# Performance work log

Measured on AMD Instinct MI355X. Metric: run time of the kernel, lower is better.

Reference implementation:

```python
import jax, jax.numpy as jnp
import numpy as np

P, NH, KEEP, TOPK = 16, 8, 0.25, 2


def _sincos_1d(embed_dim, pos):
    omega = np.arange(embed_dim // 2, dtype=np.float64)
    omega /= embed_dim / 2.0
    omega = 1.0 / 10000 ** omega
    out = np.einsum('m,d->md', pos.reshape(-1), omega)
    return np.concatenate([np.sin(out), np.cos(out)], axis=1)


def _sincos_2d(embed_dim, gh, gw):
    grid_h = np.arange(gh, dtype=np.float32)
    grid_w = np.arange(gw, dtype=np.float32)
    grid = np.stack(np.meshgrid(grid_w, grid_h), axis=0).reshape(2, -1)
    emb_h = _sincos_1d(embed_dim // 2, grid[0])  # matches original (uses grid[0])
    emb_w = _sincos_1d(embed_dim // 2, grid[1])
    return np.concatenate([emb_h, emb_w], axis=1).astype(np.float32)


def _ln(x, w, b):
    m = x.mean(-1, keepdims=True)
    v = jnp.mean((x - m) ** 2, axis=-1, keepdims=True)
    return (x - m) * jax.lax.rsqrt(v + 1e-5) * w + b


def _mha(q, kv, in_w, in_b, out_w, out_b, nh):
    D = q.shape[-1]
    dh = D // nh
    wq, wk, wv = jnp.split(in_w, 3, 0)
    bq, bk, bv = jnp.split(in_b, 3, 0)
    qq = (q @ wq.T + bq).reshape(q.shape[0], q.shape[1], nh, dh)
    kk = (kv @ wk.T + bk).reshape(kv.shape[0], kv.shape[1], nh, dh)
    vv = (kv @ wv.T + bv).reshape(kv.shape[0], kv.shape[1], nh, dh)
    att = jax.nn.softmax(jnp.einsum('bqhd,bkhd->bhqk', qq, kk) / jnp.sqrt(jnp.asarray(dh, qq.dtype)), -1)
    o = jnp.einsum('bhqk,bkhd->bqhd', att, vv).reshape(q.shape)
    return o @ out_w.T + out_b


def _moe(x, rw, rb, w1, b1, w2, b2):
    E = w1.shape[0]
    probs = jax.nn.softmax(jnp.einsum('btd,ed->bte', x, rw) + rb, -1)
    tv, ti = jax.lax.top_k(probs, TOPK)
    tw = jax.nn.softmax(tv, -1)
    comb = jnp.sum(jax.nn.one_hot(ti, E, dtype=x.dtype) * tw[..., None], axis=-2)  # [B,T,E]
    y = jnp.zeros_like(x)
    for e in range(E):  # small fixed expert count
        h = jax.nn.gelu(jnp.einsum('btd,fd->btf', x, w1[e]) + b1[e], approximate=False)
        o = jnp.einsum('btf,df->btd', h, w2[e]) + b2[e]
        y = y + comb[..., e:e + 1] * o
    return y


def reference(images, type_ids, noise, conv_w, conv_b, latents, type_emb,
              ca_in_w, ca_in_b, ca_out_w, ca_out_b, ca_ln_w, ca_ln_b,
              blk_in_w, blk_in_b, blk_out_w, blk_out_b,
              blk_ln1_w, blk_ln1_b, blk_ln2_w, blk_ln2_b,
              router_w, router_b, e_w1, e_b1, e_w2, e_b2):
    B, _, Hi, Wi = images.shape
    D = conv_w.shape[0]
    x = jax.lax.conv_general_dilated(images, conv_w, (P, P), 'VALID',
                                     dimension_numbers=('NCHW', 'OIHW', 'NCHW'))
    x = x + conv_b[None, :, None, None]
    gh, gw = Hi // P, Wi // P
    patches = x.reshape(B, D, gh * gw).transpose(0, 2, 1)  # [B,N,D]
    patches = patches + jnp.asarray(_sincos_2d(D, gh, gw))[None] + type_emb[type_ids][:, None, :]
    n = patches.shape[1]
    n_vis = max(1, int(n * KEEP))
    ids_shuffle = jnp.argsort(noise, axis=1)
    ids_keep = ids_shuffle[:, :n_vis]
    ids_mask = ids_shuffle[:, n_vis:]
    visible = jnp.take_along_axis(patches, ids_keep[..., None], axis=1)
    lat = jnp.broadcast_to(latents[None], (B,) + latents.shape)
    lat = _ln(lat + _mha(lat, visible, ca_in_w, ca_in_b, ca_out_w, ca_out_b, NH), ca_ln_w, ca_ln_b)
    L = blk_in_w.shape[0]
    for l in range(L):
        lat = _ln(lat + _mha(lat, lat, blk_in_w[l], blk_in_b[l], blk_out_w[l], blk_out_b[l], NH),
                  blk_ln1_w[l], blk_ln1_b[l])
        lat = _ln(lat + _moe(lat, router_w[l], router_b[l], e_w1[l], e_b1[l], e_w2[l], e_b2[l]),
                  blk_ln2_w[l], blk_ln2_b[l])
    return lat, ids_keep, ids_mask


def setup_inputs():
    key = jax.random.key(0)
    B, D, E, L, V = 4, 768, 8, 6, 1000
    ks = iter(jax.random.split(key, 32))

    def nrm(shape, s=0.02):
        return jax.random.normal(next(ks), shape, jnp.float32) * s

    return {
        'images': jax.random.normal(next(ks), (B, 3, 224, 224), jnp.float32),
        'type_ids': jax.random.randint(next(ks), (B,), 0, V),
        'noise': jax.random.uniform(next(ks), (B, 196), jnp.float32),
        'conv_w': nrm((D, 3, P, P)), 'conv_b': jnp.zeros((D,), jnp.float32),
        'latents': jax.random.normal(next(ks), (256, D), jnp.float32),
        'type_emb': nrm((V, D)),
        'ca_in_w': nrm((3 * D, D)), 'ca_in_b': jnp.zeros((3 * D,), jnp.float32),
        'ca_out_w': nrm((D, D)), 'ca_out_b': jnp.zeros((D,), jnp.float32),
        'ca_ln_w': jnp.ones((D,), jnp.float32), 'ca_ln_b': jnp.zeros((D,), jnp.float32),
        'blk_in_w': nrm((L, 3 * D, D)), 'blk_in_b': jnp.zeros((L, 3 * D), jnp.float32),
        'blk_out_w': nrm((L, D, D)), 'blk_out_b': jnp.zeros((L, D), jnp.float32),
        'blk_ln1_w': jnp.ones((L, D), jnp.float32), 'blk_ln1_b': jnp.zeros((L, D), jnp.float32),
        'blk_ln2_w': jnp.ones((L, D), jnp.float32), 'blk_ln2_b': jnp.zeros((L, D), jnp.float32),
        'router_w': nrm((L, E, D)), 'router_b': jnp.zeros((L, E), jnp.float32),
        'e_w1': nrm((L, E, 2 * D, D)), 'e_b1': jnp.zeros((L, E, 2 * D), jnp.float32),
        'e_w2': nrm((L, E, D, 2 * D)), 'e_b2': jnp.zeros((L, E, D), jnp.float32),
    }
```

## Files before the change

### kernel.cpp

```cpp
#include <hip/hip_runtime.h>
#include <math.h>


namespace {

typedef unsigned short u16;
constexpr int Dm  = 768;
constexpr int ML  = 256;
constexpr int BB  = 4;
constexpr int NP  = 196;
constexpr int NV  = 49;
constexpr int NE  = 8;
constexpr int FH_ = 1536;
constexpr int NL  = 6;
constexpr int NT  = 1024;

typedef __attribute__((ext_vector_type(8))) short bf16x8;
typedef __attribute__((ext_vector_type(4))) float f32x4;

__device__ __forceinline__ u16 f2bf(float f){
  union { float f; unsigned u; } v; v.f = f;
  unsigned r = v.u + 0x7fffu + ((v.u >> 16) & 1u);
  return (u16)(r >> 16);
}
__device__ __forceinline__ void pack8(const float4& a, const float4& b, bf16x8& w){
  w[0]=(short)f2bf(a.x); w[1]=(short)f2bf(a.y); w[2]=(short)f2bf(a.z); w[3]=(short)f2bf(a.w);
  w[4]=(short)f2bf(b.x); w[5]=(short)f2bf(b.y); w[6]=(short)f2bf(b.z); w[7]=(short)f2bf(b.w);
}
__device__ __forceinline__ void gload16(const void* g, void* l){
  __builtin_amdgcn_global_load_lds(
      (const __attribute__((address_space(1))) unsigned int*)g,
      (__attribute__((address_space(3))) unsigned int*)l, 16, 0, 0);
}

__device__ __forceinline__ float blk_sum(float v, float* sh){
#pragma unroll
  for (int off = 32; off; off >>= 1) v += __shfl_xor(v, off);
  int wid = threadIdx.x >> 6;
  if ((threadIdx.x & 63) == 0) sh[wid] = v;
  __syncthreads();
  v = sh[0] + sh[1] + sh[2] + sh[3];
  __syncthreads();
  return v;
}

__global__ __launch_bounds__(256) void prologue_k(
    const float* __restrict__ noise, int* __restrict__ ids,
    float* __restrict__ out_keep, float* __restrict__ out_mask,
    const float* __restrict__ images, u16* __restrict__ viscol,
    const float* __restrict__ s0, const float* __restrict__ s1,
    const float* __restrict__ s2, const float* __restrict__ s3,
    const float* __restrict__ s4, const float* __restrict__ s5,
    u16* __restrict__ d0, u16* __restrict__ d1, u16* __restrict__ d2,
    u16* __restrict__ d3, u16* __restrict__ d4, u16* __restrict__ d5)
{
  int bx = blockIdx.x, tid = threadIdx.x;
  __shared__ float shv[NP];
  __shared__ int shord[NP];
  if (bx < 4){
    int b = bx;
    if (tid < NP) shv[tid] = noise[b * NP + tid];
    __syncthreads();
    if (tid < NP){
      float x = shv[tid];
      int rank = 0;
      for (int j = 0; j < NP; j++){
        float y = shv[j];
        rank += (y < x) || (y == x && j < tid);
      }
      shord[rank] = tid;
    }
    __syncthreads();
    if (tid < NP){
      int id = shord[tid];
      ids[b * NP + tid] = id;
      if (tid < NV) out_keep[b * NV + tid] = (float)id;
      else          out_mask[b * (NP - NV) + (tid - NV)] = (float)id;
    }
    return;
  }
  if (bx < 200){
    int bv = bx - 4;
    int b = bv / NV, vq = bv % NV;
    if (tid < NP) shv[tid] = noise[b * NP + tid];
    __syncthreads();
    if (tid < NP){
      float x = shv[tid];
      int rank = 0;
      for (int j = 0; j < NP; j++){
        float y = shv[j];
        rank += (y < x) || (y == x && j < tid);
      }
      if (rank == vq) shord[0] = tid;
    }
    __syncthreads();
    int pid = shord[0];
    int ph = pid / 14, pw = pid % 14;
    int kh = tid >> 4, kw = tid & 15;
#pragma unroll
    for (int c = 0; c < 3; c++)
      viscol[(long)bv * Dm + c * 256 + tid] =
        f2bf(images[((b * 3 + c) * 224 + ph * 16 + kh) * 224 + pw * 16 + kw]);
    return;
  }
  const long c0 = 147456, c1 = 589824, c2 = 737280, c3 = 3391488, c4 = 4276224, c5 = 4325376;
  long i = (long)(bx - 200) * 256 + tid;
  long stride = (long)(gridDim.x - 200) * 256;
  for (; i < c5; i += stride){
    const float* s; u16* d; long off;
    if      (i < c0){ s = s0; d = d0; off = i; }
    else if (i < c1){ s = s1; d = d1; off = i - c0; }
    else if (i < c2){ s = s2; d = d2; off = i - c1; }
    else if (i < c3){ s = s3; d = d3; off = i - c2; }
    else if (i < c4){ s = s4; d = d4; off = i - c3; }
    else            { s = s5; d = d5; off = i - c4; }
    float4 v = *(const float4*)(s + off * 4);
    ushort4 o;
    o.x = f2bf(v.x); o.y = f2bf(v.y); o.z = f2bf(v.z); o.w = f2bf(v.w);
    *(ushort4*)(d + off * 4) = o;
  }
}

template<int MTILE, bool BF16B, bool MOE, bool GATHER, bool POSTYPE>
__global__ __launch_bounds__(256) void g2_k(
    const u16* __restrict__ A, int lda,
    const void* __restrict__ Bv, int ldb, long bSB,
    const float* __restrict__ bias, long biasE,
    float* __restrict__ Cf, u16* __restrict__ Cb, int ldc,
    int M, int N, int K, int act,
    const int* __restrict__ counts, const int* __restrict__ offsets,
    const int* __restrict__ ptok, int mbPerE,
    const int* __restrict__ ids, const int* __restrict__ type_ids,
    const float* __restrict__ type_emb)
{
  constexpr int AF = MTILE / 64;
  constexpr int MF = MTILE / 32;
  __shared__ __align__(16) short lsa[2][MTILE * 32];
  __shared__ __align__(16) short lsb[2][4096];
  int t = threadIdx.x, lane = t & 63, wid = t >> 6;
  int n0 = blockIdx.x << 7;
  int m0, cnt = 0, off = 0;
  const u16* B16 = (const u16*)Bv;
  const float* B32 = (const float*)Bv;
  const float* bb = bias;
  if (MOE){
    int e = blockIdx.y / mbPerE, mb = blockIdx.y - e * mbPerE;
    cnt = counts[e]; m0 = mb * MTILE;
    if (m0 >= cnt) return;
    off = offsets[e];
    if (BF16B) B16 += (long)e * bSB; else B32 += (long)e * bSB;
    bb += (long)e * biasE;
  } else {
    m0 = blockIdx.y * MTILE;
  }

  long aoff[AF];
#pragma unroll
  for (int i = 0; i < AF; i++){
    int idx = i * 256 + t, c = idx / MTILE, r = idx % MTILE;
    int gl = m0 + r;
    long row;
    if (MOE) row = (gl < cnt) ? (GATHER ? (long)ptok[off + gl] : (long)(off + gl))
                              : (GATHER ? (long)ptok[off] : (long)off);
    else     row = (gl < M) ? gl : 0;
    aoff[i] = row * (long)lda + c * 8;
  }
  long boff[2] = {0, 0};
  int bcol = 0, bkh = 0;
  const float* b32p = nullptr;
  if (BF16B){
#pragma unroll
    for (int i = 0; i < 2; i++){
      int idx = i * 256 + t, c = idx >> 7, r = idx & 127;
      int gc = n0 + r; if (gc >= N) gc = 0;
      boff[i] = (long)gc * ldb + c * 8;
    }
  } else {
    bcol = t >> 1; bkh = (t & 1) << 4;
    int gc = n0 + bcol; if (gc >= N) gc = N - 1;
    b32p = B32 + (long)gc * ldb + bkh;
  }

  float4 br[4];
  auto stage = [&](int buf, int k0){
#pragma unroll
    for (int i = 0; i < AF; i++)
      gload16(A + aoff[i] + k0, &lsa[buf][(i * 256 + wid * 64) * 8]);
    if (BF16B){
#pragma unroll
      for (int i = 0; i < 2; i++)
        gload16(B16 + boff[i] + k0, &lsb[buf][(i * 256 + wid * 64) * 8]);
    } else {
#pragma unroll
      for (int j = 0; j < 4; j++) br[j] = *(const float4*)(b32p + k0 + j * 4);
    }
  };
  auto bwrite = [&](int buf){
    if (!BF16B){
      bf16x8 w0, w1;
      pack8(br[0], br[1], w0); pack8(br[2], br[3], w1);
      int c0 = bkh >> 3;
      *(bf16x8*)&lsb[buf][((c0    ) * 128 + bcol) * 8] = w0;
      *(bf16x8*)&lsb[buf][((c0 + 1) * 128 + bcol) * 8] = w1;
    }
  };

  f32x4 acc[MF][4];
#pragma unroll
  for (int m = 0; m < MF; m++)
#pragma unroll
    for (int n = 0; n < 4; n++) acc[m][n] = (f32x4){0.f,0.f,0.f,0.f};

  int T = K >> 5;
  stage(0, 0);
  bwrite(0);
  __syncthreads();

  int wr = wid >> 1, wc = wid & 1, fr = lane & 15, lk = lane >> 4;
  for (int tt = 0; tt < T; tt++){
    int cur = tt & 1, nxt = cur ^ 1;
    if (tt + 1 < T) stage(nxt, (tt + 1) << 5);
    bf16x8 av[MF], bv[4];
#pragma unroll
    for (int m = 0; m < MF; m++)
      av[m] = *(const bf16x8*)&lsa[cur][(lk * MTILE + wr * (MTILE / 2) + m * 16 + fr) * 8];
#pragma unroll
    for (int n = 0; n < 4; n++)
      bv[n] = *(const bf16x8*)&lsb[cur][(lk * 128 + wc * 64 + n * 16 + fr) * 8];
#pragma unroll
    for (int m = 0; m < MF; m++)
#pragma unroll
      for (int n = 0; n < 4; n++)
        acc[m][n] = __builtin_amdgcn_mfma_f32_16x16x32_bf16(av[m], bv[n], acc[m][n], 0, 0, 0);
    if (tt + 1 < T) bwrite(nxt);
    __syncthreads();
  }

#pragma unroll
  for (int m = 0; m < MF; m++)
#pragma unroll
  for (int i = 0; i < 4; i++){
    int rl = m0 + wr * (MTILE / 2) + m * 16 + lk * 4 + i;
    bool ok = MOE ? (rl < cnt) : (rl < M);
    if (!ok) continue;
    long grow = MOE ? (long)(off + rl) : (long)rl;
    int pph = 0, ppw = 0, pty = 0;
    if (POSTYPE){
      int pb = rl / NV;
      int pid = ids[pb * NP + rl % NV];
      pph = pid / 14; ppw = pid % 14;
      pty = type_ids[pb];
    }
#pragma unroll
    for (int n = 0; n < 4; n++){
      int col = n0 + wc * 64 + n * 16 + fr;
      if (col >= N) continue;
      float v = acc[m][n][i] + bb[col];
      if (act) v = 0.5f * v * (1.0f + erff(v * 0.70710678118654752f));
      if (POSTYPE){
        int q = col % 192, sect = col / 192;
        float omega = powf(10000.0f, -(float)q / 192.0f);
        float arg = (sect < 2 ? (float)ppw : (float)pph) * omega;
        float pos = ((sect & 1) == 0) ? sinf(arg) : cosf(arg);
        v += pos + type_emb[(long)pty * Dm + col];
      }
      if (Cf) Cf[grow * (long)ldc + col] = v;
      if (Cb) Cb[grow * (long)ldc + col] = f2bf(v);
    }
  }
}

template<int KVCAP>
__global__ __launch_bounds__(256) void flash_k(
    const u16* __restrict__ Qp, int ldq, int qBatchRows,
    const u16* __restrict__ Kp, int ldk,
    const u16* __restrict__ Vp, int ldv, int kvBatchRows,
    int qCol0, int kCol0, int vCol0,
    int kvLen, u16* __restrict__ Ob)
{
  constexpr int NF   = KVCAP / 16;
  constexpr int HALF = (KVCAP > 128) ? 128 : KVCAP;
  constexpr int NHF  = KVCAP / HALF;

  __shared__ __align__(16) char sm[49152];
  short* smQ  = (short*)sm;
  short* smK0 = (short*)(sm + 12288);
  short* smK1 = (short*)(sm + 12288 + 4 * KVCAP * 16);
  short* smP  = (short*)sm;
  short* smVT = (short*)(sm + 64 * HALF * 2);

  int t = threadIdx.x, lane = t & 63, wid = t >> 6;
  int fr = lane & 15, lk = lane >> 4;
  int qt = blockIdx.x, z = blockIdx.y, b = z >> 3, h = z & 7;
  int qRow0 = b * qBatchRows + qt * 64;
  int kvRow0 = b * kvBatchRows;
  int oRow0 = b * 256 + qt * 64;
  int qCol = qCol0 + h * 96, kCol = kCol0 + h * 96, vCol = vCol0 + h * 96;
  int wq0 = wid * 16;

#pragma unroll
  for (int i = 0; i < 3; i++){
    int idx = i * 256 + t, c = idx >> 6, r = idx & 63;
    *(bf16x8*)&smQ[idx * 8] = *(const bf16x8*)&Qp[(long)(qRow0 + r) * ldq + qCol + c * 8];
  }
  auto stageK = [&](int k0c, short* dst){
#pragma unroll
    for (int i = 0; i < (4 * KVCAP) / 256; i++){
      int idx = i * 256 + t, c = idx / KVCAP, col = idx % KVCAP;
      int kv = col < kvLen ? col : kvLen - 1;
      *(bf16x8*)&dst[idx * 8] =
        *(const bf16x8*)&Kp[(long)(kvRow0 + kv) * ldk + kCol + (k0c * 4 + c) * 8];
    }
  };
  stageK(0, smK0);
  __syncthreads();

  f32x4 acc[NF];
#pragma unroll
  for (int n = 0; n < NF; n++) acc[n] = (f32x4){0.f,0.f,0.f,0.f};

  for (int k0c = 0; k0c < 3; k0c++){
    short* curK = (k0c & 1) ? smK1 : smK0;
    if (k0c < 2) stageK(k0c + 1, (k0c & 1) ? smK0 : smK1);
    bf16x8 av = *(const bf16x8*)&smQ[((k0c * 4 + lk) * 64 + wq0 + fr) * 8];
#pragma unroll
    for (int n = 0; n < NF; n++){
      bf16x8 bv = *(const bf16x8*)&curK[(lk * KVCAP + n * 16 + fr) * 8];
      acc[n] = __builtin_amdgcn_mfma_f32_16x16x32_bf16(av, bv, acc[n], 0, 0, 0);
    }
    __syncthreads();
  }

  const float scl = 0.10206207261596577f;
  float rinv[4];
#pragma unroll
  for (int i = 0; i < 4; i++){
    float mx = -3e38f;
#pragma unroll
    for (int n = 0; n < NF; n++){
      float v = acc[n][i] * scl;
      if (n * 16 + fr >= kvLen) v = -3e38f;
      acc[n][i] = v;
      mx = fmaxf(mx, v);
    }
#pragma unroll
    for (int s = 1; s < 16; s <<= 1) mx = fmaxf(mx, __shfl_xor(mx, s));
    float sum = 0.f;
#pragma unroll
    for (int n = 0; n < NF; n++){
      float p = __expf(acc[n][i] - mx);
      acc[n][i] = p;
      sum += p;
    }
#pragma unroll
    for (int s = 1; s < 16; s <<= 1) sum += __shfl_xor(sum, s);
    rinv[i] = 1.0f / sum;
  }

  f32x4 acco[6];
#pragma unroll
  for (int n = 0; n < 6; n++) acco[n] = (f32x4){0.f,0.f,0.f,0.f};

  for (int hf = 0; hf < NHF; hf++){
    if (hf) __syncthreads();
#pragma unroll
    for (int np = 0; np < HALF / 16; np++){
      int n = hf * (HALF / 16) + np;
#pragma unroll
      for (int i = 0; i < 4; i++){
        int row = wq0 + lk * 4 + i;
        int cl = np * 16 + fr;
        smP[((cl >> 3) * 64 + row) * 8 + (cl & 7)] = (short)f2bf(acc[n][i]);
      }
    }
    constexpr int G = (HALF * 96 / 8) / 256;
#pragma unroll
    for (int g = 0; g < G; g++){
      int flat = g * 256 + t;
      int kvl = flat / 12, dblk = (flat % 12) * 8;
      int kvg = hf * HALF + kvl;
      int kva = kvg < kvLen ? kvg : kvLen - 1;
      bf16x8 v = *(const bf16x8*)&Vp[(long)(kvRow0 + kva) * ldv + vCol + dblk];
      bool zz = kvg >= kvLen;
#pragma unroll
      for (int j = 0; j < 8; j++)
        smVT[((kvl >> 3) * 96 + dblk + j) * 8 + (kvl & 7)] = zz ? (short)0 : v[j];
    }
    __syncthreads();
#pragma unroll
    for (int kk = 0; kk < HALF / 32; kk++){
      bf16x8 pa = *(const bf16x8*)&smP[((kk * 4 + lk) * 64 + wq0 + fr) * 8];
#pragma unroll
      for (int n = 0; n < 6; n++){
        bf16x8 bv = *(const bf16x8*)&smVT[((kk * 4 + lk) * 96 + n * 16 + fr) * 8];
        acco[n] = __builtin_amdgcn_mfma_f32_16x16x32_bf16(pa, bv, acco[n], 0, 0, 0);
      }
    }
  }

#pragma unroll
  for (int n = 0; n < 6; n++)
#pragma unroll
  for (int i = 0; i < 4; i++){
    int row = oRow0 + wq0 + lk * 4 + i;
    Ob[(long)row * 768 + h * 96 + n * 16 + fr] = f2bf(acco[n][i] * rinv[i]);
  }
}

__global__ __launch_bounds__(256) void add_ln_k(
    const float* __restrict__ X, const float* __restrict__ R, int rMod,
    const float* __restrict__ w, const float* __restrict__ b,
    float* __restrict__ outf, u16* __restrict__ outb)
{
  int row = blockIdx.x;
  int rrow = rMod ? (row % rMod) : row;
  __shared__ float sh[4];
  float x[3];
#pragma unroll
  for (int i = 0; i < 3; i++){
    int d = threadIdx.x + (i << 8);
    x[i] = X[(long)row * Dm + d] + R[(long)rrow * Dm + d];
  }
  float s = blk_sum(x[0] + x[1] + x[2], sh);
  float mean = s * (1.0f / 768.0f);
  float vs = 0.f;
#pragma unroll
  for (int i = 0; i < 3; i++){ float tt = x[i] - mean; vs += tt * tt; }
  vs = blk_sum(vs, sh);
  float rstd = rsqrtf(vs * (1.0f / 768.0f) + 1e-5f);
#pragma unroll
  for (int i = 0; i < 3; i++){
    int d = threadIdx.x + (i << 8);
    float o = (x[i] - mean) * rstd * w[d] + b[d];
    outf[(long)row * Dm + d] = o;
    if (outb) outb[(long)row * Dm + d] = f2bf(o);
  }
}

__global__ __launch_bounds__(256) void router_k(
    const float* __restrict__ lat, const float* __restrict__ rw, const float* __restrict__ rb,
    int* __restrict__ top_idx, float* __restrict__ top_w)
{
  int t = blockIdx.x, tid = threadIdx.x;
  int e = tid >> 5, lane = tid & 31;
  const float* x = lat + (long)t * Dm;
  const float* w = rw + (long)e * Dm;
  float s = 0.f;
  for (int j = 0; j < 24; j++){ int d = lane + 32 * j; s += x[d] * w[d]; }
#pragma unroll
  for (int off = 16; off; off >>= 1) s += __shfl_xor(s, off);
  __shared__ float lg[NE];
  if (lane == 0) lg[e] = s + rb[e];
  __syncthreads();
  if (tid == 0){
    float m = -1e30f;
    for (int i = 0; i < NE; i++) m = fmaxf(m, lg[i]);
    float p[NE]; float se = 0.f;
    for (int i = 0; i < NE; i++){ p[i] = __expf(lg[i] - m); se += p[i]; }
    float inv = 1.0f / se;
    int i0 = 0, i1 = -1; float v0 = -1.f, v1 = -1.f;
    for (int i = 0; i < NE; i++){
      float pi = p[i] * inv;
      if (pi > v0){ v1 = v0; i1 = i0; v0 = pi; i0 = i; }
      else if (pi > v1){ v1 = pi; i1 = i; }
    }
    float w0 = 1.0f / (1.0f + __expf(v1 - v0));
    top_idx[2 * t] = i0; top_idx[2 * t + 1] = i1;
    top_w[2 * t] = w0;   top_w[2 * t + 1] = 1.0f - w0;
  }
}

__global__ __launch_bounds__(256) void scatter_k(
    const int* __restrict__ top_idx, int* __restrict__ counts, int* __restrict__ offsets,
    int* __restrict__ ptok, int* __restrict__ posmap)
{
  __shared__ int cnt[NE], cur[NE];
  int tid = threadIdx.x;
  if (tid < NE) cnt[tid] = 0;
  __syncthreads();
  for (int t = tid; t < NT; t += 256){
    atomicAdd(&cnt[top_idx[2 * t]], 1);
    atomicAdd(&cnt[top_idx[2 * t + 1]], 1);
  }
  __syncthreads();
  if (tid == 0){
    int o = 0;
    for (int e = 0; e < NE; e++){ offsets[e] = o; cur[e] = o; counts[e] = cnt[e]; o += cnt[e]; }
  }
  __syncthreads();
  for (int t = tid; t < NT; t += 256){
#pragma unroll
    for (int sidx = 0; sidx < 2; sidx++){
      int e = top_idx[2 * t + sidx];
      int pos = atomicAdd(&cur[e], 1);
      ptok[pos] = t;
      posmap[2 * t + sidx] = pos;
    }
  }
}

__global__ __launch_bounds__(256) void moe_combine_ln_k(
    const float* __restrict__ OBuf, const int* __restrict__ posmap, const float* __restrict__ topw,
    const float* __restrict__ latin, const float* __restrict__ w, const float* __restrict__ b,
    float* __restrict__ outf, u16* __restrict__ outb)
{
  int t = blockIdx.x;
  int p0 = posmap[2 * t], p1 = posmap[2 * t + 1];
  float w0 = topw[2 * t], w1 = topw[2 * t + 1];
  __shared__ float sh[4];
  float x[3];
#pragma unroll
  for (int i = 0; i < 3; i++){
    int d = threadIdx.x + (i << 8);
    x[i] = w0 * OBuf[(long)p0 * Dm + d] + w1 * OBuf[(long)p1 * Dm + d] + latin[(long)t * Dm + d];
  }
  float s = blk_sum(x[0] + x[1] + x[2], sh);
  float mean = s * (1.0f / 768.0f);
  float vs = 0.f;
#pragma unroll
  for (int i = 0; i < 3; i++){ float tt = x[i] - mean; vs += tt * tt; }
  vs = blk_sum(vs, sh);
  float rstd = rsqrtf(vs * (1.0f / 768.0f) + 1e-5f);
#pragma unroll
  for (int i = 0; i < 3; i++){
    int d = threadIdx.x + (i << 8);
    float o = (x[i] - mean) * rstd * w[d] + b[d];
    outf[(long)t * Dm + d] = o;
    if (outb) outb[(long)t * Dm + d] = f2bf(o);
  }
}

}

extern "C" void kernel_launch(void* const* d_in, const int* in_sizes, int n_in,
                              void* d_out, int out_size, void* d_ws, size_t ws_size,
                              hipStream_t stream)
{
  (void)in_sizes; (void)n_in; (void)out_size; (void)ws_size;
  const float* images    = (const float*)d_in[0];
  const int*   type_ids  = (const int*)d_in[1];
  const float* noise     = (const float*)d_in[2];
  const float* conv_w    = (const float*)d_in[3];
  const float* conv_b    = (const float*)d_in[4];
  const float* latents   = (const float*)d_in[5];
  const float* type_emb  = (const float*)d_in[6];
  const float* ca_in_w   = (const float*)d_in[7];
  const float* ca_in_b   = (const float*)d_in[8];
  const float* ca_out_w  = (const float*)d_in[9];
  const float* ca_out_b  = (const float*)d_in[10];
  const float* ca_ln_w   = (const float*)d_in[11];
  const float* ca_ln_b   = (const float*)d_in[12];
  const float* blk_in_w  = (const float*)d_in[13];
  const float* blk_in_b  = (const float*)d_in[14];
  const float* blk_out_w = (const float*)d_in[15];
  const float* blk_out_b = (const float*)d_in[16];
  const float* blk_ln1_w = (const float*)d_in[17];
  const float* blk_ln1_b = (const float*)d_in[18];
  const float* blk_ln2_w = (const float*)d_in[19];
  const float* blk_ln2_b = (const float*)d_in[20];
  const float* router_w  = (const float*)d_in[21];
  const float* router_b  = (const float*)d_in[22];
  const float* e_w1      = (const float*)d_in[23];
  const float* e_b1      = (const float*)d_in[24];
  const float* e_w2      = (const float*)d_in[25];
  const float* e_b2      = (const float*)d_in[26];

  char* W = (char*)d_ws;
  float* lat   = (float*)(W + 0);
  float* tmp   = (float*)(W + 3145728);
  float* obuf  = (float*)(W + 6291456);
  float* topw  = (float*)(W + 13185024);
  int*   ids      = (int*)(W + 13193216);
  int*   top_idx  = (int*)(W + 13197312);
  int*   posmap   = (int*)(W + 13205504);
  int*   ptok     = (int*)(W + 13213696);
  int*   counts   = (int*)(W + 13221888);
  int*   offsets  = (int*)(W + 13221952);
  u16* lat_bf    = (u16*)(W + 13258752);
  u16* ao_bf     = (u16*)(W + 14831616);
  u16* qkv_bf    = (u16*)(W + 16404480);
  u16* h_bf      = (u16*)(W + 21123072);
  u16* viscol_bf = (u16*)(W + 27414528);
  u16* vis_bf    = (u16*)(W + 27715584);
  u16* qq_bf     = (u16*)(W + 28016640);
  u16* kkvv_bf   = (u16*)(W + 28409856);
  u16* lat0_bf   = (u16*)(W + 29011968);
  u16* convw_bf  = (u16*)(W + 29405184);
  u16* caw_bf    = (u16*)(W + 30584832);
  u16* caow_bf   = (u16*)(W + 34123776);
  u16* blkin_bf  = (u16*)(W + 35303424);
  u16* blkout_bf = (u16*)(W + 56537088);

  float* out      = (float*)d_out;
  float* out_lat  = out;
  float* out_keep = out + (long)NT * Dm;
  float* out_mask = out_keep + BB * NV;

  dim3 blk(256);

  prologue_k<<<2248, blk, 0, stream>>>(
      noise, ids, out_keep, out_mask, images, viscol_bf,
      conv_w, ca_in_w, ca_out_w, blk_in_w, blk_out_w, latents,
      convw_bf, caw_bf, caow_bf, blkin_bf, blkout_bf, lat0_bf);

  g2_k<64,true,false,false,true><<<dim3(6, 4), blk, 0, stream>>>(
      viscol_bf, Dm, convw_bf, Dm, 0, conv_b, 0,
      nullptr, vis_bf, Dm, BB * NV, Dm, Dm, 0,
      nullptr, nullptr, nullptr, 1, ids, type_ids, type_emb);

  g2_k<64,true,false,false,false><<<dim3(6, 4), blk, 0, stream>>>(
      lat0_bf, Dm, caw_bf, Dm, 0, ca_in_b, 0,
      nullptr, qq_bf, Dm, ML, Dm, Dm, 0,
      nullptr, nullptr, nullptr, 1, nullptr, nullptr, nullptr);
  g2_k<64,true,false,false,false><<<dim3(12, 4), blk, 0, stream>>>(
      vis_bf, Dm, caw_bf + 768 * 768, Dm, 0, ca_in_b + 768, 0,
      nullptr, kkvv_bf, 1536, BB * NV, 1536, Dm, 0,
      nullptr, nullptr, nullptr, 1, nullptr, nullptr, nullptr);
  flash_k<64><<<dim3(4, 32), blk, 0, stream>>>(
      qq_bf, Dm, 0, kkvv_bf, 1536, kkvv_bf, 1536, NV, 0, 0, 768, NV, ao_bf);
  g2_k<64,true,false,false,false><<<dim3(6, 16), blk, 0, stream>>>(
      ao_bf, Dm, caow_bf, Dm, 0, ca_out_b, 0,
      tmp, nullptr, Dm, NT, Dm, Dm, 0,
      nullptr, nullptr, nullptr, 1, nullptr, nullptr, nullptr);
  add_ln_k<<<NT, blk, 0, stream>>>(tmp, latents, ML, ca_ln_w, ca_ln_b, lat, lat_bf);

  for (int l = 0; l < NL; l++){
    g2_k<64,true,false,false,false><<<dim3(18, 16), blk, 0, stream>>>(
        lat_bf, Dm, blkin_bf + (long)l * 2304 * 768, Dm, 0, blk_in_b + (long)l * 2304, 0,
        nullptr, qkv_bf, 2304, NT, 2304, Dm, 0,
        nullptr, nullptr, nullptr, 1, nullptr, nullptr, nullptr);
    flash_k<256><<<dim3(4, 32), blk, 0, stream>>>(
        qkv_bf, 2304, ML, qkv_bf, 2304, qkv_bf, 2304, ML, 0, 768, 1536, ML, ao_bf);
    g2_k<64,true,false,false,false><<<dim3(6, 16), blk, 0, stream>>>(
        ao_bf, Dm, blkout_bf + (long)l * 768 * 768, Dm, 0, blk_out_b + (long)l * 768, 0,
        tmp, nullptr, Dm, NT, Dm, Dm, 0,
        nullptr, nullptr, nullptr, 1, nullptr, nullptr, nullptr);
    add_ln_k<<<NT, blk, 0, stream>>>(tmp, lat, 0,
        blk_ln1_w + (long)l * 768, blk_ln1_b + (long)l * 768, lat, lat_bf);
    router_k<<<NT, blk, 0, stream>>>(lat, router_w + (long)l * NE * Dm,
                                     router_b + (long)l * NE, top_idx, topw);
    scatter_k<<<1, blk, 0, stream>>>(top_idx, counts, offsets, ptok, posmap);
    g2_k<64,false,true,true,false><<<dim3(12, 128), blk, 0, stream>>>(
        lat_bf, Dm, e_w1 + (long)l * NE * FH_ * Dm, Dm, (long)FH_ * Dm,
        e_b1 + (long)l * NE * FH_, FH_,
        nullptr, h_bf, FH_, 0, FH_, Dm, 1,
        counts, offsets, ptok, 16, nullptr, nullptr, nullptr);
    g2_k<64,false,true,false,false><<<dim3(6, 128), blk, 0, stream>>>(
        h_bf, FH_, e_w2 + (long)l * NE * Dm * FH_, FH_, (long)Dm * FH_,
        e_b2 + (long)l * NE * Dm, Dm,
        obuf, nullptr, Dm, 0, Dm, FH_, 0,
        counts, offsets, ptok, 16, nullptr, nullptr, nullptr);
    moe_combine_ln_k<<<NT, blk, 0, stream>>>(obuf, posmap, topw, lat,
        blk_ln2_w + (long)l * 768, blk_ln2_b + (long)l * 768,
        (l == NL - 1) ? out_lat : lat, (l == NL - 1) ? nullptr : lat_bf);
  }
}
```

Baseline: 1.303 ms.

## Fuse MoE router and token scatter into add-LN kernel with fixed-capacity expert slots

The router logits, softmax/top-2 selection and token dispatch now run inside the post-attention add+LayerNorm kernel, removing the separate router and single-block scatter launches. Scatter uses global atomics into fixed-capacity per-expert slots (CAP=2048), with counters zeroed once in the prologue for all layers. The expert GEMM grids grow to cover 32 tiles per expert so they can span the padded capacity, which launches more blocks that may exit early. Token order within each expert becomes nondeterministic, and buffers are relocated to fit the larger padded layout.

```diff
diff --git a/kernel.cpp b/kernel.cpp
--- a/kernel.cpp
+++ b/kernel.cpp
@@ -14,6 +14,7 @@
 constexpr int FH_ = 1536;
 constexpr int NL  = 6;
 constexpr int NT  = 1024;
+constexpr int CAP = 2048;
 
 typedef __attribute__((ext_vector_type(8))) short bf16x8;
 typedef __attribute__((ext_vector_type(4))) float f32x4;
@@ -52,13 +53,18 @@
     const float* __restrict__ s2, const float* __restrict__ s3,
     const float* __restrict__ s4, const float* __restrict__ s5,
     u16* __restrict__ d0, u16* __restrict__ d1, u16* __restrict__ d2,
-    u16* __restrict__ d3, u16* __restrict__ d4, u16* __restrict__ d5)
+    u16* __restrict__ d3, u16* __restrict__ d4, u16* __restrict__ d5,
+    int* __restrict__ gcnt, int* __restrict__ offsets)
 {
   int bx = blockIdx.x, tid = threadIdx.x;
   __shared__ float shv[NP];
   __shared__ int shord[NP];
   if (bx < 4){
     int b = bx;
+    if (b == 0){
+      if (tid >= 200 && tid < 200 + NL * NE) gcnt[tid - 200] = 0;
+      if (tid >= 248 && tid < 256) offsets[tid - 248] = (tid - 248) * CAP;
+    }
     if (tid < NP) shv[tid] = noise[b * NP + tid];
     __syncthreads();
     if (tid < NP){
@@ -410,11 +416,15 @@
 __global__ __launch_bounds__(256) void add_ln_k(
     const float* __restrict__ X, const float* __restrict__ R, int rMod,
     const float* __restrict__ w, const float* __restrict__ b,
-    float* __restrict__ outf, u16* __restrict__ outb)
+    float* __restrict__ outf, u16* __restrict__ outb,
+    const float* __restrict__ rw, const float* __restrict__ rb,
+    int* __restrict__ ptok, int* __restrict__ posmap,
+    float* __restrict__ topw, int* __restrict__ gcnt)
 {
   int row = blockIdx.x;
   int rrow = rMod ? (row % rMod) : row;
   __shared__ float sh[4];
+  __shared__ float lg8[NE][4];
   float x[3];
 #pragma unroll
   for (int i = 0; i < 3; i++){
@@ -428,73 +438,57 @@
   for (int i = 0; i < 3; i++){ float tt = x[i] - mean; vs += tt * tt; }
   vs = blk_sum(vs, sh);
   float rstd = rsqrtf(vs * (1.0f / 768.0f) + 1e-5f);
+  float o[3];
 #pragma unroll
   for (int i = 0; i < 3; i++){
     int d = threadIdx.x + (i << 8);
-    float o = (x[i] - mean) * rstd * w[d] + b[d];
-    outf[(long)row * Dm + d] = o;
-    if (outb) outb[(long)row * Dm + d] = f2bf(o);
-  }
-}
-
-__global__ __launch_bounds__(256) void router_k(
-    const float* __restrict__ lat, const float* __restrict__ rw, const float* __restrict__ rb,
-    int* __restrict__ top_idx, float* __restrict__ top_w)
-{
-  int t = blockIdx.x, tid = threadIdx.x;
-  int e = tid >> 5, lane = tid & 31;
-  const float* x = lat + (long)t * Dm;
-  const float* w = rw + (long)e * Dm;
-  float s = 0.f;
-  for (int j = 0; j < 24; j++){ int d = lane + 32 * j; s += x[d] * w[d]; }
-#pragma unroll
-  for (int off = 16; off; off >>= 1) s += __shfl_xor(s, off);
-  __shared__ float lg[NE];
-  if (lane == 0) lg[e] = s + rb[e];
-  __syncthreads();
-  if (tid == 0){
-    float m = -1e30f;
-    for (int i = 0; i < NE; i++) m = fmaxf(m, lg[i]);
-    float p[NE]; float se = 0.f;
-    for (int i = 0; i < NE; i++){ p[i] = __expf(lg[i] - m); se += p[i]; }
-    float inv = 1.0f / se;
-    int i0 = 0, i1 = -1; float v0 = -1.f, v1 = -1.f;
-    for (int i = 0; i < NE; i++){
-      float pi = p[i] * inv;
-      if (pi > v0){ v1 = v0; i1 = i0; v0 = pi; i0 = i; }
-      else if (pi > v1){ v1 = pi; i1 = i; }
-    }
-    float w0 = 1.0f / (1.0f + __expf(v1 - v0));
-    top_idx[2 * t] = i0; top_idx[2 * t + 1] = i1;
-    top_w[2 * t] = w0;   top_w[2 * t + 1] = 1.0f - w0;
-  }
-}
-
-__global__ __launch_bounds__(256) void scatter_k(
-    const int* __restrict__ top_idx, int* __restrict__ counts, int* __restrict__ offsets,
-    int* __restrict__ ptok, int* __restrict__ posmap)
-{
-  __shared__ int cnt[NE], cur[NE];
-  int tid = threadIdx.x;
-  if (tid < NE) cnt[tid] = 0;
-  __syncthreads();
-  for (int t = tid; t < NT; t += 256){
-    atomicAdd(&cnt[top_idx[2 * t]], 1);
-    atomicAdd(&cnt[top_idx[2 * t + 1]], 1);
-  }
-  __syncthreads();
-  if (tid == 0){
-    int o = 0;
-    for (int e = 0; e < NE; e++){ offsets[e] = o; cur[e] = o; counts[e] = cnt[e]; o += cnt[e]; }
-  }
-  __syncthreads();
-  for (int t = tid; t < NT; t += 256){
-#pragma unroll
-    for (int sidx = 0; sidx < 2; sidx++){
-      int e = top_idx[2 * t + sidx];
-      int pos = atomicAdd(&cur[e], 1);
-      ptok[pos] = t;
-      posmap[2 * t + sidx] = pos;
+    o[i] = (x[i] - mean) * rstd * w[d] + b[d];
+    outf[(long)row * Dm + d] = o[i];
+    if (outb) outb[(long)row * Dm + d] = f2bf(o[i]);
+  }
+  if (rw){
+    float pe[NE];
+#pragma unroll
+    for (int e = 0; e < NE; e++){
+      const float* rwe = rw + (long)e * Dm;
+      pe[e] = o[0] * rwe[threadIdx.x]
+            + o[1] * rwe[threadIdx.x + 256]
+            + o[2] * rwe[threadIdx.x + 512];
+    }
+#pragma unroll
+    for (int e = 0; e < NE; e++)
+#pragma unroll
+      for (int s2 = 32; s2; s2 >>= 1) pe[e] += __shfl_xor(pe[e], s2);
+    int wid2 = threadIdx.x >> 6;
+    if ((threadIdx.x & 63) == 0)
+#pragma unroll
+      for (int e = 0; e < NE; e++) lg8[e][wid2] = pe[e];
+    __syncthreads();
+    if (threadIdx.x == 0){
+      float lg[NE];
+      float m = -1e30f;
+      for (int e = 0; e < NE; e++){
+        lg[e] = lg8[e][0] + lg8[e][1] + lg8[e][2] + lg8[e][3] + rb[e];
+        m = fmaxf(m, lg[e]);
+      }
+      float p[NE]; float se = 0.f;
+      for (int e = 0; e < NE; e++){ p[e] = __expf(lg[e] - m); se += p[e]; }
+      float inv = 1.0f / se;
+      int i0 = 0, i1 = -1; float v0 = -1.f, v1 = -1.f;
+      for (int e = 0; e < NE; e++){
+        float pi = p[e] * inv;
+        if (pi > v0){ v1 = v0; i1 = i0; v0 = pi; i0 = e; }
+        else if (pi > v1){ v1 = pi; i1 = e; }
+      }
+      float w0 = 1.0f / (1.0f + __expf(v1 - v0));
+      topw[2 * row] = w0; topw[2 * row + 1] = 1.0f - w0;
+      int e0 = i0, e1 = i1;
+      int pos0 = atomicAdd(&gcnt[e0], 1);
+      ptok[e0 * CAP + pos0] = row;
+      posmap[2 * row] = e0 * CAP + pos0;
+      int pos1 = atomicAdd(&gcnt[e1], 1);
+      ptok[e1 * CAP + pos1] = row;
+      posmap[2 * row + 1] = e1 * CAP + pos1;
     }
   }
 }
@@ -568,28 +562,27 @@
   char* W = (char*)d_ws;
   float* lat   = (float*)(W + 0);
   float* tmp   = (float*)(W + 3145728);
-  float* obuf  = (float*)(W + 6291456);
   float* topw  = (float*)(W + 13185024);
   int*   ids      = (int*)(W + 13193216);
-  int*   top_idx  = (int*)(W + 13197312);
   int*   posmap   = (int*)(W + 13205504);
-  int*   ptok     = (int*)(W + 13213696);
-  int*   counts   = (int*)(W + 13221888);
-  int*   offsets  = (int*)(W + 13221952);
-  u16* lat_bf    = (u16*)(W + 13258752);
-  u16* ao_bf     = (u16*)(W + 14831616);
-  u16* qkv_bf    = (u16*)(W + 16404480);
-  u16* h_bf      = (u16*)(W + 21123072);
-  u16* viscol_bf = (u16*)(W + 27414528);
-  u16* vis_bf    = (u16*)(W + 27715584);
-  u16* qq_bf     = (u16*)(W + 28016640);
-  u16* kkvv_bf   = (u16*)(W + 28409856);
-  u16* lat0_bf   = (u16*)(W + 29011968);
-  u16* convw_bf  = (u16*)(W + 29405184);
-  u16* caw_bf    = (u16*)(W + 30584832);
-  u16* caow_bf   = (u16*)(W + 34123776);
-  u16* blkin_bf  = (u16*)(W + 35303424);
-  u16* blkout_bf = (u16*)(W + 56537088);
+  int*   gcnt     = (int*)(W + 13221888);
+  int*   offsets  = (int*)(W + 13222144);
+  int*   ptok     = (int*)(W + 13222400);
+  u16* lat_bf    = (u16*)(W + 13303808);
+  u16* ao_bf     = (u16*)(W + 14876672);
+  u16* qkv_bf    = (u16*)(W + 16449536);
+  u16* viscol_bf = (u16*)(W + 27459584);
+  u16* vis_bf    = (u16*)(W + 27760640);
+  u16* qq_bf     = (u16*)(W + 28061696);
+  u16* kkvv_bf   = (u16*)(W + 28454912);
+  u16* lat0_bf   = (u16*)(W + 29057024);
+  u16* convw_bf  = (u16*)(W + 29450240);
+  u16* caw_bf    = (u16*)(W + 30629888);
+  u16* caow_bf   = (u16*)(W + 34168832);
+  u16* blkin_bf  = (u16*)(W + 35348480);
+  u16* blkout_bf = (u16*)(W + 56582144);
+  u16* h_bf      = (u16*)(W + 63660032);
+  float* obuf    = (float*)(W + 113991680);
 
   float* out      = (float*)d_out;
   float* out_lat  = out;
@@ -601,7 +594,8 @@
   prologue_k<<<2248, blk, 0, stream>>>(
       noise, ids, out_keep, out_mask, images, viscol_bf,
       conv_w, ca_in_w, ca_out_w, blk_in_w, blk_out_w, latents,
-      convw_bf, caw_bf, caow_bf, blkin_bf, blkout_bf, lat0_bf);
+      convw_bf, caw_bf, caow_bf, blkin_bf, blkout_bf, lat0_bf,
+      gcnt, offsets);
 
   g2_k<64,true,false,false,true><<<dim3(6, 4), blk, 0, stream>>>(
       viscol_bf, Dm, convw_bf, Dm, 0, conv_b, 0,
@@ -622,7 +616,8 @@
       ao_bf, Dm, caow_bf, Dm, 0, ca_out_b, 0,
       tmp, nullptr, Dm, NT, Dm, Dm, 0,
       nullptr, nullptr, nullptr, 1, nullptr, nullptr, nullptr);
-  add_ln_k<<<NT, blk, 0, stream>>>(tmp, latents, ML, ca_ln_w, ca_ln_b, lat, lat_bf);
+  add_ln_k<<<NT, blk, 0, stream>>>(tmp, latents, ML, ca_ln_w, ca_ln_b, lat, lat_bf,
+                                   nullptr, nullptr, nullptr, nullptr, nullptr, nullptr);
 
   for (int l = 0; l < NL; l++){
     g2_k<64,true,false,false,false><<<dim3(18, 16), blk, 0, stream>>>(
@@ -636,20 +631,19 @@
         tmp, nullptr, Dm, NT, Dm, Dm, 0,
         nullptr, nullptr, nullptr, 1, nullptr, nullptr, nullptr);
     add_ln_k<<<NT, blk, 0, stream>>>(tmp, lat, 0,
-        blk_ln1_w + (long)l * 768, blk_ln1_b + (long)l * 768, lat, lat_bf);
-    router_k<<<NT, blk, 0, stream>>>(lat, router_w + (long)l * NE * Dm,
-                                     router_b + (long)l * NE, top_idx, topw);
-    scatter_k<<<1, blk, 0, stream>>>(top_idx, counts, offsets, ptok, posmap);
-    g2_k<64,false,true,true,false><<<dim3(12, 128), blk, 0, stream>>>(
+        blk_ln1_w + (long)l * 768, blk_ln1_b + (long)l * 768, lat, lat_bf,
+        router_w + (long)l * NE * Dm, router_b + (long)l * NE,
+        ptok, posmap, topw, gcnt + l * NE);
+    g2_k<64,false,true,true,false><<<dim3(12, 256), blk, 0, stream>>>(
         lat_bf, Dm, e_w1 + (long)l * NE * FH_ * Dm, Dm, (long)FH_ * Dm,
         e_b1 + (long)l * NE * FH_, FH_,
         nullptr, h_bf, FH_, 0, FH_, Dm, 1,
-        counts, offsets, ptok, 16, nullptr, nullptr, nullptr);
-    g2_k<64,false,true,false,false><<<dim3(6, 128), blk, 0, stream>>>(
+        gcnt + l * NE, offsets, ptok, 32, nullptr, nullptr, nullptr);
+    g2_k<64,false,true,false,false><<<dim3(6, 256), blk, 0, stream>>>(
         h_bf, FH_, e_w2 + (long)l * NE * Dm * FH_, FH_, (long)Dm * FH_,
         e_b2 + (long)l * NE * Dm, Dm,
         obuf, nullptr, Dm, 0, Dm, FH_, 0,
-        counts, offsets, ptok, 16, nullptr, nullptr, nullptr);
+        gcnt + l * NE, offsets, ptok, 32, nullptr, nullptr, nullptr);
     moe_combine_ln_k<<<NT, blk, 0, stream>>>(obuf, posmap, topw, lat,
         blk_ln2_w + (long)l * 768, blk_ln2_b + (long)l * 768,
         (l == NL - 1) ? out_lat : lat, (l == NL - 1) ? nullptr : lat_bf);
```

New measurement: 1.591 ms. 22.0% more time.
